# Kernel tuning notes

Hardware: AMD Instinct MI355X
Metric: run time of the kernel (lower is better)

The kernel has to match this reference:

```python
import jax, jax.numpy as jnp
import numpy as np

B, S1, S2, H1, H2, HID = 8, 512, 512, 128, 128, 128

def setup_inputs() -> dict:
    key = jax.random.key(0)
    ks = jax.random.split(key, 8)
    return {
        "query": jax.random.normal(ks[0], (B, S1, H1), jnp.float32),
        "key": jax.random.normal(ks[1], (B, S2, H2), jnp.float32),
        "value": jax.random.normal(ks[2], (B, S2, H2), jnp.float32),
        "q_mask": jax.random.randint(ks[3], (B, S1), 0, 2, jnp.int32),
        "k_mask": jax.random.randint(ks[4], (B, S2), 0, 2, jnp.int32),
        # init_weights: Linear weight ~ N(0, 0.01), bias = 0
        "W1": jax.random.normal(ks[5], (HID, H1 + H2), jnp.float32) * 0.01,
        "b1": jnp.zeros((HID,), jnp.float32),
        "W2": jax.random.normal(ks[6], (1, HID), jnp.float32) * 0.01,
        "b2": jnp.zeros((1,), jnp.float32),
    }

def reference(query, key, value, q_mask, k_mask, W1, b1, W2, b2):
    h1 = query.shape[-1]
    # Linear on concat([q,k]) == q @ W1[:, :h1].T + k @ W1[:, h1:].T + b1
    qp = jnp.einsum('bsd,hd->bsh', query, W1[:, :h1]) + b1   # [B,S1,HID]
    kp = jnp.einsum('btd,hd->bth', key, W1[:, h1:])          # [B,S2,HID]
    h = jax.nn.relu(qp[:, :, None, :] + kp[:, None, :, :])   # [B,S1,S2,HID]
    s = jnp.einsum('bsth,h->bst', h, W2[0]) + b2[0]          # [B,S1,S2]
    mask = (q_mask[:, :, None] * k_mask[:, None, :]) > 0     # [B,S1,S2]
    A = jnp.where(mask, jnp.exp(s), 0.0)                     # masked_fill(-inf).exp()
    A_sum = jnp.clip(jnp.sum(A, axis=-1, keepdims=True), 2e-15, None)
    attn = A / A_sum
    return jnp.einsum('bst,btd->bsd', attn, value)           # [B,S1,H2]
```

## Files before the change

### kernel.cpp

```cpp
#include <hip/hip_runtime.h>

#define S 512
#define H 128
#define NROW 4096
#define TI 8

__global__ __launch_bounds__(256) void proj_kernel(
    const float* __restrict__ query, const float* __restrict__ key,
    const float* __restrict__ W1, const float* __restrict__ b1,
    float* __restrict__ qp, float* __restrict__ kp)
{
  __shared__ float w1t[128][130];
  const int bid = blockIdx.x;
  const bool isq = bid < 128;
  const float* __restrict__ src = isq ? query : key;
  const int rbase = (isq ? bid : bid - 128) * 32;
  const int off = isq ? 0 : 128;
  const int tid = threadIdx.x;

  for (int idx = tid; idx < 128 * 32; idx += 256) {
    const int d4 = idx & 31, h = idx >> 5;
    const float4 v = *(const float4*)(W1 + h * 256 + off + d4 * 4);
    w1t[d4 * 4 + 0][h] = v.x;
    w1t[d4 * 4 + 1][h] = v.y;
    w1t[d4 * 4 + 2][h] = v.z;
    w1t[d4 * 4 + 3][h] = v.w;
  }
  __syncthreads();

  const int w = __builtin_amdgcn_readfirstlane(tid >> 6);
  const int lane = tid & 63;
  const int r0 = rbase + w * 8;

  float acc[8][2];
  float2 bv = make_float2(0.f, 0.f);
  if (isq) bv = *(const float2*)(b1 + 2 * lane);
  #pragma unroll
  for (int r = 0; r < 8; r++) { acc[r][0] = bv.x; acc[r][1] = bv.y; }

  for (int dc = 0; dc < 128; dc += 8) {
    float qs[8][8];
    #pragma unroll
    for (int r = 0; r < 8; r++) {
      const float* sp = src + (size_t)(r0 + r) * H + dc;
      #pragma unroll
      for (int u = 0; u < 8; u++) qs[r][u] = sp[u];
    }
    #pragma unroll
    for (int dd = 0; dd < 8; dd++) {
      const float2 wv = *(const float2*)&w1t[dc + dd][2 * lane];
      #pragma unroll
      for (int r = 0; r < 8; r++) {
        acc[r][0] = __builtin_fmaf(qs[r][dd], wv.x, acc[r][0]);
        acc[r][1] = __builtin_fmaf(qs[r][dd], wv.y, acc[r][1]);
      }
    }
  }
  float* __restrict__ dst = isq ? qp : kp;
  #pragma unroll
  for (int r = 0; r < 8; r++) {
    *(float2*)(dst + (size_t)(r0 + r) * H + 2 * lane) =
        make_float2(acc[r][0], acc[r][1]);
  }
}

__global__ __launch_bounds__(256) void attn_kernel(
    const float* __restrict__ qp, const float* __restrict__ kp,
    const float* __restrict__ value, const int* __restrict__ q_mask,
    const int* __restrict__ k_mask, const float* __restrict__ W2,
    const float* __restrict__ b2,
    float* __restrict__ nump, float* __restrict__ denp)
{
  __shared__ float aT[4][64][12];
  __shared__ float numk[TI][132];
  __shared__ float denk[TI];

  const int it = blockIdx.x;
  const int jh = blockIdx.y;
  const int r0 = it * TI;
  const int b  = r0 >> 9;
  const int tid = threadIdx.x;
  const int w = __builtin_amdgcn_readfirstlane(tid >> 6);
  const int lane = tid & 63;
  const int jl = (jh << 8) + (w << 6) + lane;
  const int jg = (b << 9) + jl;
  const int km = k_mask[jg];
  const float* __restrict__ kprow = kp + (size_t)jg * H;
  const float b2v = b2[0];

  float s[TI];
  #pragma unroll
  for (int i = 0; i < TI; i++) s[i] = 0.f;

  for (int hc = 0; hc < H; hc += 16) {
    float kr[16];
    #pragma unroll
    for (int u = 0; u < 4; u++) {
      const float4 v4 = *(const float4*)(kprow + hc + u * 4);
      kr[u*4+0] = v4.x; kr[u*4+1] = v4.y; kr[u*4+2] = v4.z; kr[u*4+3] = v4.w;
    }
    float w2r[16];
    #pragma unroll
    for (int u = 0; u < 16; u++) w2r[u] = W2[hc + u];
    #pragma unroll
    for (int i = 0; i < TI; i++) {
      const float* __restrict__ qrow = qp + (size_t)(r0 + i) * H + hc;
      #pragma unroll
      for (int u = 0; u < 16; u++) {
        float t = fmaxf(qrow[u] + kr[u], 0.f);
        s[i] = __builtin_fmaf(t, w2r[u], s[i]);
      }
    }
  }

  float a[TI], den[TI];
  #pragma unroll
  for (int i = 0; i < TI; i++) {
    const int qm = q_mask[r0 + i];
    a[i] = (km > 0 && qm > 0) ? __expf(s[i] + b2v) : 0.f;
  }
  #pragma unroll
  for (int i = 0; i < TI; i++) {
    float d = a[i];
    #pragma unroll
    for (int m = 32; m >= 1; m >>= 1) d += __shfl_xor(d, m, 64);
    den[i] = d;
  }
  #pragma unroll
  for (int i = 0; i < TI; i++) aT[w][lane][i] = a[i];
  __syncthreads();

  const int lj = lane >> 5, lh = lane & 31;
  float nr[TI][4];
  #pragma unroll
  for (int i = 0; i < TI; i++) { nr[i][0]=0.f; nr[i][1]=0.f; nr[i][2]=0.f; nr[i][3]=0.f; }
  const float* __restrict__ vbase =
      value + ((size_t)b * S + (jh << 8) + (w << 6)) * H;

  for (int js = 0; js < 32; js++) {
    const int j = js * 2 + lj;
    const float4 vv = *(const float4*)(vbase + (size_t)j * H + lh * 4);
    float av[TI];
    { const float4 t0 = *(const float4*)&aT[w][j][0];
      const float4 t1 = *(const float4*)&aT[w][j][4];
      av[0]=t0.x; av[1]=t0.y; av[2]=t0.z; av[3]=t0.w;
      av[4]=t1.x; av[5]=t1.y; av[6]=t1.z; av[7]=t1.w; }
    #pragma unroll
    for (int i = 0; i < TI; i++) {
      nr[i][0] = __builtin_fmaf(av[i], vv.x, nr[i][0]);
      nr[i][1] = __builtin_fmaf(av[i], vv.y, nr[i][1]);
      nr[i][2] = __builtin_fmaf(av[i], vv.z, nr[i][2]);
      nr[i][3] = __builtin_fmaf(av[i], vv.w, nr[i][3]);
    }
  }
  #pragma unroll
  for (int i = 0; i < TI; i++) {
    #pragma unroll
    for (int k = 0; k < 4; k++) nr[i][k] += __shfl_xor(nr[i][k], 32, 64);
  }

  for (int r = 0; r < 4; r++) {
    if (w == r) {
      if (lj == 0) {
        #pragma unroll
        for (int i = 0; i < TI; i++) {
          float4* p = (float4*)&numk[i][lh * 4];
          if (r == 0) {
            *p = make_float4(nr[i][0], nr[i][1], nr[i][2], nr[i][3]);
          } else {
            float4 t = *p;
            t.x += nr[i][0]; t.y += nr[i][1]; t.z += nr[i][2]; t.w += nr[i][3];
            *p = t;
          }
        }
      }
      if (lane == 0) {
        #pragma unroll
        for (int i = 0; i < TI; i++)
          denk[i] = (r == 0) ? den[i] : denk[i] + den[i];
      }
    }
    __syncthreads();
  }

  {
    const int i = tid >> 5, seg = tid & 31;
    const float4 v = *(const float4*)&numk[i][seg * 4];
    float* dst = nump + ((size_t)jh * NROW + (size_t)(r0 + i)) * H + seg * 4;
    *(float4*)dst = v;
    if (tid < TI) denp[jh * NROW + r0 + tid] = denk[tid];
  }
}

__global__ __launch_bounds__(256) void finalize_kernel(
    const float* __restrict__ nump, const float* __restrict__ denp,
    float* __restrict__ out)
{
  const int idx = blockIdx.x * 256 + threadIdx.x;
  const int row = idx >> 5;
  const float4 a = *(const float4*)(nump + (size_t)idx * 4);
  const float4 c = *(const float4*)(nump + (size_t)NROW * H + (size_t)idx * 4);
  const float d = denp[row] + denp[NROW + row];
  const float inv = 1.f / fmaxf(d, 2e-15f);
  float4 o;
  o.x = (a.x + c.x) * inv; o.y = (a.y + c.y) * inv;
  o.z = (a.z + c.z) * inv; o.w = (a.w + c.w) * inv;
  *(float4*)(out + (size_t)idx * 4) = o;
}

extern "C" void kernel_launch(void* const* d_in, const int* in_sizes, int n_in,
                              void* d_out, int out_size, void* d_ws, size_t ws_size,
                              hipStream_t stream)
{
  (void)in_sizes; (void)n_in; (void)out_size; (void)ws_size;
  const float* query  = (const float*)d_in[0];
  const float* key    = (const float*)d_in[1];
  const float* value  = (const float*)d_in[2];
  const int*   q_mask = (const int*)d_in[3];
  const int*   k_mask = (const int*)d_in[4];
  const float* W1     = (const float*)d_in[5];
  const float* b1     = (const float*)d_in[6];
  const float* W2     = (const float*)d_in[7];
  const float* b2     = (const float*)d_in[8];
  float* out = (float*)d_out;

  float* ws   = (float*)d_ws;
  float* qp   = ws;
  float* kp   = ws + (size_t)NROW * H;
  float* nump = ws + (size_t)2 * NROW * H;
  float* denp = ws + (size_t)4 * NROW * H;

  proj_kernel<<<256, 256, 0, stream>>>(query, key, W1, b1, qp, kp);
  attn_kernel<<<dim3(512, 2), 256, 0, stream>>>(qp, kp, value, q_mask, k_mask,
                                                W2, b2, nump, denp);
  finalize_kernel<<<512, 256, 0, stream>>>(nump, denp, out);
}
```

Measured before the change: 121.2 us.

## Use packed fp16 dot2 for score MLP and fuse finalize into attention

The projection kernel now stores qp, kp and W2 as packed half2 values. The attention kernel computes relu(q+k)·W2 with packed fp16 adds, max and fdot2 accumulating into fp32, which halves the ALU work and memory traffic of the dominant S1×S2×HID loop. The attention block now covers all 512 keys with 512 threads, so the cross-half reduction and the separate finalize kernel are dropped and the output is written directly. The cost is fp16 rounding of the projected features before exp, which may affect accuracy tolerance.

```diff
diff --git a/kernel.cpp b/kernel.cpp
--- a/kernel.cpp
+++ b/kernel.cpp
@@ -5,10 +5,15 @@
 #define NROW 4096
 #define TI 8
 
+typedef _Float16 h2v __attribute__((ext_vector_type(2)));
+#define BCH(x) __builtin_bit_cast(h2v, (x))
+
 __global__ __launch_bounds__(256) void proj_kernel(
     const float* __restrict__ query, const float* __restrict__ key,
     const float* __restrict__ W1, const float* __restrict__ b1,
-    float* __restrict__ qp, float* __restrict__ kp)
+    const float* __restrict__ W2,
+    unsigned* __restrict__ qph, unsigned* __restrict__ kph,
+    unsigned* __restrict__ w2h)
 {
   __shared__ float w1t[128][130];
   const int bid = blockIdx.x;
@@ -18,6 +23,13 @@
   const int off = isq ? 0 : 128;
   const int tid = threadIdx.x;
 
+  if (bid == 0 && tid < 64) {
+    h2v p;
+    p.x = (_Float16)W2[2 * tid];
+    p.y = (_Float16)W2[2 * tid + 1];
+    w2h[tid] = __builtin_bit_cast(unsigned, p);
+  }
+
   for (int idx = tid; idx < 128 * 32; idx += 256) {
     const int d4 = idx & 31, h = idx >> 5;
     const float4 v = *(const float4*)(W1 + h * 256 + off + d4 * 4);
@@ -56,64 +68,77 @@
       }
     }
   }
-  float* __restrict__ dst = isq ? qp : kp;
+  unsigned* __restrict__ dst = isq ? qph : kph;
   #pragma unroll
   for (int r = 0; r < 8; r++) {
-    *(float2*)(dst + (size_t)(r0 + r) * H + 2 * lane) =
-        make_float2(acc[r][0], acc[r][1]);
+    h2v p;
+    p.x = (_Float16)acc[r][0];
+    p.y = (_Float16)acc[r][1];
+    dst[(size_t)(r0 + r) * 64 + lane] = __builtin_bit_cast(unsigned, p);
   }
 }
 
-__global__ __launch_bounds__(256) void attn_kernel(
-    const float* __restrict__ qp, const float* __restrict__ kp,
-    const float* __restrict__ value, const int* __restrict__ q_mask,
-    const int* __restrict__ k_mask, const float* __restrict__ W2,
-    const float* __restrict__ b2,
-    float* __restrict__ nump, float* __restrict__ denp)
+__global__ __launch_bounds__(512) void attn_kernel(
+    const unsigned* __restrict__ qph, const unsigned* __restrict__ kph,
+    const unsigned* __restrict__ w2h, const float* __restrict__ value,
+    const int* __restrict__ q_mask, const int* __restrict__ k_mask,
+    const float* __restrict__ b2, float* __restrict__ out)
 {
-  __shared__ float aT[4][64][12];
-  __shared__ float numk[TI][132];
-  __shared__ float denk[TI];
+  union __align__(16) SMU {
+    float aT[8][64][12];
+    float numk[8][TI][128];
+  };
+  __shared__ SMU sm;
+  __shared__ float denk[8][TI];
 
   const int it = blockIdx.x;
-  const int jh = blockIdx.y;
   const int r0 = it * TI;
-  const int b  = r0 >> 9;
+  const int b = r0 >> 9;
   const int tid = threadIdx.x;
   const int w = __builtin_amdgcn_readfirstlane(tid >> 6);
   const int lane = tid & 63;
-  const int jl = (jh << 8) + (w << 6) + lane;
+  const int jl = (w << 6) + lane;
   const int jg = (b << 9) + jl;
   const int km = k_mask[jg];
-  const float* __restrict__ kprow = kp + (size_t)jg * H;
+  const unsigned* __restrict__ kprow = kph + (size_t)jg * 64;
   const float b2v = b2[0];
+  const h2v hz = {};
 
   float s[TI];
   #pragma unroll
   for (int i = 0; i < TI; i++) s[i] = 0.f;
 
-  for (int hc = 0; hc < H; hc += 16) {
-    float kr[16];
-    #pragma unroll
-    for (int u = 0; u < 4; u++) {
-      const float4 v4 = *(const float4*)(kprow + hc + u * 4);
-      kr[u*4+0] = v4.x; kr[u*4+1] = v4.y; kr[u*4+2] = v4.z; kr[u*4+3] = v4.w;
-    }
-    float w2r[16];
-    #pragma unroll
-    for (int u = 0; u < 16; u++) w2r[u] = W2[hc + u];
+  for (int hc = 0; hc < 64; hc += 16) {
+    h2v kr[16];
+    {
+      const uint4* k4 = (const uint4*)(kprow + hc);
+      const uint4 a0 = k4[0], a1 = k4[1], a2 = k4[2], a3 = k4[3];
+      kr[0]  = BCH(a0.x); kr[1]  = BCH(a0.y); kr[2]  = BCH(a0.z); kr[3]  = BCH(a0.w);
+      kr[4]  = BCH(a1.x); kr[5]  = BCH(a1.y); kr[6]  = BCH(a1.z); kr[7]  = BCH(a1.w);
+      kr[8]  = BCH(a2.x); kr[9]  = BCH(a2.y); kr[10] = BCH(a2.z); kr[11] = BCH(a2.w);
+      kr[12] = BCH(a3.x); kr[13] = BCH(a3.y); kr[14] = BCH(a3.z); kr[15] = BCH(a3.w);
+    }
+    h2v w2c[16];
+    #pragma unroll
+    for (int u = 0; u < 16; u++) w2c[u] = BCH(w2h[hc + u]);
+
     #pragma unroll
     for (int i = 0; i < TI; i++) {
-      const float* __restrict__ qrow = qp + (size_t)(r0 + i) * H + hc;
+      const unsigned* __restrict__ qrow =
+          qph + (size_t)(r0 + i) * 64 + hc;
+      unsigned qu[16];
+      #pragma unroll
+      for (int u = 0; u < 16; u++) qu[u] = qrow[u];
       #pragma unroll
       for (int u = 0; u < 16; u++) {
-        float t = fmaxf(qrow[u] + kr[u], 0.f);
-        s[i] = __builtin_fmaf(t, w2r[u], s[i]);
+        h2v t = BCH(qu[u]) + kr[u];
+        t = __builtin_elementwise_max(t, hz);
+        s[i] = __builtin_amdgcn_fdot2(t, w2c[u], s[i], false);
       }
     }
   }
 
-  float a[TI], den[TI];
+  float a[TI];
   #pragma unroll
   for (int i = 0; i < TI; i++) {
     const int qm = q_mask[r0 + i];
@@ -124,10 +149,10 @@
     float d = a[i];
     #pragma unroll
     for (int m = 32; m >= 1; m >>= 1) d += __shfl_xor(d, m, 64);
-    den[i] = d;
-  }
-  #pragma unroll
-  for (int i = 0; i < TI; i++) aT[w][lane][i] = a[i];
+    if (lane == 0) denk[w][i] = d;
+  }
+  *(float4*)&sm.aT[w][lane][0] = make_float4(a[0], a[1], a[2], a[3]);
+  *(float4*)&sm.aT[w][lane][4] = make_float4(a[4], a[5], a[6], a[7]);
   __syncthreads();
 
   const int lj = lane >> 5, lh = lane & 31;
@@ -135,14 +160,14 @@
   #pragma unroll
   for (int i = 0; i < TI; i++) { nr[i][0]=0.f; nr[i][1]=0.f; nr[i][2]=0.f; nr[i][3]=0.f; }
   const float* __restrict__ vbase =
-      value + ((size_t)b * S + (jh << 8) + (w << 6)) * H;
+      value + ((size_t)b * S + (w << 6)) * H;
 
   for (int js = 0; js < 32; js++) {
     const int j = js * 2 + lj;
     const float4 vv = *(const float4*)(vbase + (size_t)j * H + lh * 4);
     float av[TI];
-    { const float4 t0 = *(const float4*)&aT[w][j][0];
-      const float4 t1 = *(const float4*)&aT[w][j][4];
+    { const float4 t0 = *(const float4*)&sm.aT[w][j][0];
+      const float4 t1 = *(const float4*)&sm.aT[w][j][4];
       av[0]=t0.x; av[1]=t0.y; av[2]=t0.z; av[3]=t0.w;
       av[4]=t1.x; av[5]=t1.y; av[6]=t1.z; av[7]=t1.w; }
     #pragma unroll
@@ -159,53 +184,26 @@
     for (int k = 0; k < 4; k++) nr[i][k] += __shfl_xor(nr[i][k], 32, 64);
   }
 
-  for (int r = 0; r < 4; r++) {
-    if (w == r) {
-      if (lj == 0) {
-        #pragma unroll
-        for (int i = 0; i < TI; i++) {
-          float4* p = (float4*)&numk[i][lh * 4];
-          if (r == 0) {
-            *p = make_float4(nr[i][0], nr[i][1], nr[i][2], nr[i][3]);
-          } else {
-            float4 t = *p;
-            t.x += nr[i][0]; t.y += nr[i][1]; t.z += nr[i][2]; t.w += nr[i][3];
-            *p = t;
-          }
-        }
-      }
-      if (lane == 0) {
-        #pragma unroll
-        for (int i = 0; i < TI; i++)
-          denk[i] = (r == 0) ? den[i] : denk[i] + den[i];
-      }
-    }
-    __syncthreads();
-  }
-
-  {
-    const int i = tid >> 5, seg = tid & 31;
-    const float4 v = *(const float4*)&numk[i][seg * 4];
-    float* dst = nump + ((size_t)jh * NROW + (size_t)(r0 + i)) * H + seg * 4;
-    *(float4*)dst = v;
-    if (tid < TI) denp[jh * NROW + r0 + tid] = denk[tid];
-  }
-}
-
-__global__ __launch_bounds__(256) void finalize_kernel(
-    const float* __restrict__ nump, const float* __restrict__ denp,
-    float* __restrict__ out)
-{
-  const int idx = blockIdx.x * 256 + threadIdx.x;
-  const int row = idx >> 5;
-  const float4 a = *(const float4*)(nump + (size_t)idx * 4);
-  const float4 c = *(const float4*)(nump + (size_t)NROW * H + (size_t)idx * 4);
-  const float d = denp[row] + denp[NROW + row];
+  __syncthreads();
+  if (lane < 32) {
+    #pragma unroll
+    for (int i = 0; i < TI; i++)
+      *(float4*)&sm.numk[w][i][lane * 4] =
+          make_float4(nr[i][0], nr[i][1], nr[i][2], nr[i][3]);
+  }
+  __syncthreads();
+
+  const int ii = tid >> 6;
+  const int h0 = (tid & 63) * 2;
+  float nx = 0.f, ny = 0.f, d = 0.f;
+  #pragma unroll
+  for (int ww = 0; ww < 8; ww++) {
+    const float2 t = *(const float2*)&sm.numk[ww][ii][h0];
+    nx += t.x; ny += t.y;
+    d += denk[ww][ii];
+  }
   const float inv = 1.f / fmaxf(d, 2e-15f);
-  float4 o;
-  o.x = (a.x + c.x) * inv; o.y = (a.y + c.y) * inv;
-  o.z = (a.z + c.z) * inv; o.w = (a.w + c.w) * inv;
-  *(float4*)(out + (size_t)idx * 4) = o;
+  *(float2*)(out + (size_t)(r0 + ii) * H + h0) = make_float2(nx * inv, ny * inv);
 }
 
 extern "C" void kernel_launch(void* const* d_in, const int* in_sizes, int n_in,
@@ -224,14 +222,12 @@
   const float* b2     = (const float*)d_in[8];
   float* out = (float*)d_out;
 
-  float* ws   = (float*)d_ws;
-  float* qp   = ws;
-  float* kp   = ws + (size_t)NROW * H;
-  float* nump = ws + (size_t)2 * NROW * H;
-  float* denp = ws + (size_t)4 * NROW * H;
-
-  proj_kernel<<<256, 256, 0, stream>>>(query, key, W1, b1, qp, kp);
-  attn_kernel<<<dim3(512, 2), 256, 0, stream>>>(qp, kp, value, q_mask, k_mask,
-                                                W2, b2, nump, denp);
-  finalize_kernel<<<512, 256, 0, stream>>>(nump, denp, out);
+  unsigned* ws  = (unsigned*)d_ws;
+  unsigned* qph = ws;
+  unsigned* kph = ws + (size_t)NROW * 64;
+  unsigned* w2h = kph + (size_t)NROW * 64;
+
+  proj_kernel<<<256, 256, 0, stream>>>(query, key, W1, b1, W2, qph, kph, w2h);
+  attn_kernel<<<512, 512, 0, stream>>>(qph, kph, w2h, value, q_mask, k_mask,
+                                       b2, out);
 }
```

Measured after the change: 111.9 us. 7.7% less time.
